# Kernel tuning notes

Hardware: AMD Instinct MI355X
Metric: run time of the kernel (lower is better)

The kernel has to match this reference:

```python
import jax, jax.numpy as jnp
import numpy as np

B, T, D = 4, 4096, 1024
N_DOCS, TOP_K, HEADS = 4096, 8, 4
EPS = 1e-12  # matches F.normalize default eps


def setup_inputs() -> dict:
    key = jax.random.key(0)
    ks = jax.random.split(key, 14)
    f = jnp.float32
    s = D ** -0.5
    return {
        "x": jax.random.normal(ks[0], (B, T, D), f),
        "hex_weights": jax.random.normal(ks[1], (B, T, 64), f),
        "doc_keys": jax.random.normal(ks[2], (N_DOCS, 64), f) * 0.1,
        "doc_values": jax.random.normal(ks[3], (N_DOCS, D), f) * 0.1,
        "Wq_hex": jax.random.normal(ks[4], (64, 64), f) * 0.125,
        "Wq": jax.random.normal(ks[5], (D, D), f) * s,
        "Wk": jax.random.normal(ks[6], (D, D), f) * s,
        "Wv": jax.random.normal(ks[7], (D, D), f) * s,
        "bq": jnp.zeros((D,), f),
        "bk": jnp.zeros((D,), f),
        "bv": jnp.zeros((D,), f),
        "Wo": jax.random.normal(ks[8], (D, D), f) * s,
        "bo": jnp.zeros((D,), f),
        "W_doc": jax.random.normal(ks[9], (D, D), f) * s,
        "gate": jnp.zeros((1,), f),
    }


def _l2norm(v):
    return v / jnp.maximum(jnp.linalg.norm(v, axis=-1, keepdims=True), EPS)


def reference(x, hex_weights, doc_keys, doc_values, Wq_hex, Wq, Wk, Wv,
              bq, bk, bv, Wo, bo, W_doc, gate):
    # --- retrieve: cosine similarity in 64-dim hexagram space ---
    q = hex_weights @ Wq_hex                      # (B,T,64)
    sim = jnp.einsum('bth,nh->btn', _l2norm(q), _l2norm(doc_keys))  # (B,T,N_DOCS)
    top_scores, top_idx = jax.lax.top_k(sim, TOP_K)  # (B,T,K)

    # --- gather + softmax-weighted combine ---
    doc_vals = doc_values[top_idx]                # (B,T,K,D) irregular gather
    attn_w = jax.nn.softmax(top_scores, axis=-1)  # (B,T,K)
    retrieved = jnp.einsum('btk,btkd->btd', attn_w, doc_vals)  # (B,T,D)
    doc_context = retrieved @ W_doc               # (B,T,D)

    # --- degenerate cross-attention: q len 1, kv len 1 per token ---
    # softmax over a single key is exactly 1, so attention output = v;
    # q/k projections contribute nothing (and have zero gradient), matching torch.
    v = doc_context @ Wv + bv                     # (B,T,D)
    out = v @ Wo + bo                             # out_proj

    return x + jax.nn.sigmoid(gate) * out
```

## Files before the change

### kernel.cpp

```cpp
#include <hip/hip_runtime.h>
#include <math.h>

#define NTOK  16384
#define DDIM  1024
#define NDOCS 4096
#define NSLICE 8
#define SLICE (NDOCS/NSLICE)
#define TOPL  6
#define KPT   64
#define MN20  (1u<<20)

typedef __attribute__((ext_vector_type(8))) short short8;
typedef __attribute__((ext_vector_type(4))) float f32x4;

__device__ __forceinline__ float b2f(unsigned short u){
  union { unsigned int i; float f; } v; v.i = ((unsigned int)u) << 16; return v.f;
}
__device__ __forceinline__ unsigned short f2b(float f){
  union { float f; unsigned int i; } v; v.f = f;
  unsigned int r = v.i + 0x7fffu + ((v.i >> 16) & 1u);
  return (unsigned short)(r >> 16);
}
__device__ __forceinline__ void gld16(const void* g, void* l){
  __builtin_amdgcn_global_load_lds(
      (const __attribute__((address_space(1))) void*)g,
      (__attribute__((address_space(3))) void*)l, 16, 0, 0);
}
__device__ __forceinline__ void kinsert(unsigned int* keys, unsigned int key){
  #pragma unroll
  for (int k = TOPL-1; k >= 1; --k){
    unsigned int lo = keys[k-1] < key ? keys[k-1] : key;
    keys[k] = keys[k] > lo ? keys[k] : lo;
  }
  keys[0] = keys[0] > key ? keys[0] : key;
}
__device__ __forceinline__ void ceswap(unsigned int& a, unsigned int& b){
  unsigned int mx = a > b ? a : b, mn = a > b ? b : a; a = mx; b = mn;
}
__device__ __forceinline__ void bitonic8(unsigned int* c){
  ceswap(c[0],c[4]); ceswap(c[1],c[5]); ceswap(c[2],c[6]); ceswap(c[3],c[7]);
  ceswap(c[0],c[2]); ceswap(c[1],c[3]); ceswap(c[4],c[6]); ceswap(c[5],c[7]);
  ceswap(c[0],c[1]); ceswap(c[2],c[3]); ceswap(c[4],c[5]); ceswap(c[6],c[7]);
}

__global__ __launch_bounds__(256)
void prep_kernel(const float* __restrict__ dvals, unsigned short* __restrict__ dv16,
                 const float* __restrict__ Wdoc,  unsigned short* __restrict__ wd16,
                 const float* __restrict__ Wv,    unsigned short* __restrict__ T1,
                 const float* __restrict__ Wo,    unsigned short* __restrict__ T2,
                 const float* __restrict__ bv, const float* __restrict__ bo,
                 float* __restrict__ bc){
  __shared__ unsigned short t[32][33];
  __shared__ float part[4][64];
  int bx = blockIdx.x, tid = threadIdx.x;
  if (bx < 5120){
    const float* in        = bx < 4096 ? dvals : Wdoc;
    unsigned short* outp   = bx < 4096 ? dv16  : wd16;
    size_t base = (size_t)(bx < 4096 ? bx : bx - 4096) * 1024;
    size_t i = base + (size_t)tid * 4;
    float4 v = *(const float4*)(in + i);
    ushort4 o; o.x = f2b(v.x); o.y = f2b(v.y); o.z = f2b(v.z); o.w = f2b(v.w);
    *(ushort4*)(outp + i) = o;
  } else if (bx < 7168){
    int b = bx - 5120;
    const float* in      = b < 1024 ? Wv : Wo;
    unsigned short* outp = b < 1024 ? T1 : T2;
    b &= 1023;
    int c0 = (b & 31) * 32, r0 = (b >> 5) * 32;
    int lc = tid & 31, lr = tid >> 5;
    #pragma unroll
    for (int i = 0; i < 4; i++){
      int r = lr + i*8;
      t[r][lc] = f2b(in[(size_t)(r0 + r)*DDIM + c0 + lc]);
    }
    __syncthreads();
    #pragma unroll
    for (int i = 0; i < 4; i++){
      int r = lr + i*8;
      outp[(size_t)(c0 + r)*DDIM + r0 + lc] = t[lc][r];
    }
  } else {
    int b = bx - 7168;
    int lane = tid & 63, w = tid >> 6;
    int n = b * 64 + lane;
    float acc = 0.f;
    int k0 = w * 256;
    for (int k = k0; k < k0 + 256; k++)
      acc += bv[k] * Wo[(size_t)k*DDIM + n];
    part[w][lane] = acc;
    __syncthreads();
    if (w == 0)
      bc[n] = part[0][lane] + part[1][lane] + part[2][lane] + part[3][lane] + bo[n];
  }
}

__global__ __launch_bounds__(256)
void norm_kernel(const float* __restrict__ hexw, const float* __restrict__ Wq,
                 float* __restrict__ qn, const float* __restrict__ dkeys,
                 float* __restrict__ dkn, unsigned short* __restrict__ dkn16s){
  __shared__ float Wsh[64*64];
  __shared__ float hx[4][64];
  int bx = blockIdx.x, tid = threadIdx.x;
  int w = tid >> 6, j = tid & 63;
  if (bx < 4096){
    #pragma unroll
    for (int i = 0; i < 16; i++){ int e = tid + i*256; Wsh[e] = Wq[e]; }
    int t = bx * 4 + w;
    hx[w][j] = hexw[(size_t)t*64 + j];
    __syncthreads();
    float s = 0.f;
    #pragma unroll
    for (int h = 0; h < 64; h++) s += hx[w][h] * Wsh[h*64 + j];
    float ss = s*s;
    #pragma unroll
    for (int off = 32; off >= 1; off >>= 1) ss += __shfl_xor(ss, off, 64);
    qn[(size_t)t*64 + j] = s / fmaxf(sqrtf(ss), 1e-12f);
  } else {
    int t = (bx - 4096) * 4 + w;
    float v = dkeys[(size_t)t*64 + j];
    float ss = v*v;
    #pragma unroll
    for (int off = 32; off >= 1; off >>= 1) ss += __shfl_xor(ss, off, 64);
    float o = v / fmaxf(sqrtf(ss), 1e-12f);
    dkn[(size_t)t*64 + j] = o;
    dkn16s[((size_t)(t >> 5) << 11) + ((j >> 3) << 8) + ((t & 31) << 3) + (j & 7)] = f2b(o);
  }
}

__global__ __launch_bounds__(256)
void topk_part(const float* __restrict__ qn, const unsigned short* __restrict__ dkn16s,
               unsigned int* __restrict__ kbuf){
  __shared__ __align__(16) unsigned short buf[2][2048];
  int tid  = threadIdx.x;
  int wv   = tid >> 6;
  int lane = tid & 63;
  int tl   = lane & 15;
  int g    = lane >> 4;
  int token = blockIdx.x*64 + wv*16 + tl;
  int dbase = blockIdx.y * SLICE;
  int T0    = dbase >> 5;

  const float* qrow = qn + (size_t)token*64 + g*8;
  float4 u0 = *(const float4*)(qrow);
  float4 u1 = *(const float4*)(qrow + 4);
  float4 v0 = *(const float4*)(qrow + 32);
  float4 v1 = *(const float4*)(qrow + 36);
  short8 q0 = (short8){(short)f2b(u0.x),(short)f2b(u0.y),(short)f2b(u0.z),(short)f2b(u0.w),
                       (short)f2b(u1.x),(short)f2b(u1.y),(short)f2b(u1.z),(short)f2b(u1.w)};
  short8 q1 = (short8){(short)f2b(v0.x),(short)f2b(v0.y),(short)f2b(v0.z),(short)f2b(v0.w),
                       (short)f2b(v1.x),(short)f2b(v1.y),(short)f2b(v1.z),(short)f2b(v1.w)};

  unsigned int keysA[TOPL], keysB[TOPL];
  #pragma unroll
  for (int k = 0; k < TOPL; k++){ keysA[k] = 0u; keysB[k] = 0u; }
  const unsigned int HI = 0xFFFF0000u;
  unsigned int idlow0 = 4095u - (unsigned)(dbase + g*4);

  gld16(dkn16s + ((size_t)T0 << 11) + wv*512 + lane*8, &buf[0][wv*512]);
  __syncthreads();

  #pragma unroll 2
  for (int it = 0; it < SLICE/32; ++it){
    int cur = it & 1;
    if (it < SLICE/32 - 1)
      gld16(dkn16s + ((size_t)(T0 + it + 1) << 11) + wv*512 + lane*8,
            &buf[cur ^ 1][wv*512]);

    const unsigned short* bp = &buf[cur][0];
    short8 a0 = *(const short8*)(bp + g*256        + tl*8);
    short8 a1 = *(const short8*)(bp + (g+4)*256    + tl*8);
    short8 b0 = *(const short8*)(bp + g*256 + 128  + tl*8);
    short8 b1 = *(const short8*)(bp + (g+4)*256 + 128 + tl*8);

    f32x4 accA = (f32x4){3.0f, 3.0f, 3.0f, 3.0f};
    f32x4 accB = (f32x4){3.0f, 3.0f, 3.0f, 3.0f};
    accA = __builtin_amdgcn_mfma_f32_16x16x32_bf16(a0, q0, accA, 0, 0, 0);
    accB = __builtin_amdgcn_mfma_f32_16x16x32_bf16(b0, q0, accB, 0, 0, 0);
    accA = __builtin_amdgcn_mfma_f32_16x16x32_bf16(a1, q1, accA, 0, 0, 0);
    accB = __builtin_amdgcn_mfma_f32_16x16x32_bf16(b1, q1, accB, 0, 0, 0);

    unsigned int ibA = idlow0 - (unsigned)(it*32);
    unsigned int ibB = ibA - 16u;
    #pragma unroll
    for (int r = 0; r < 4; ++r){
      unsigned int kA = (((__float_as_uint(accA[r]) << 8) - 0xC0000000u) & HI)
                      | (ibA - (unsigned)r);
      unsigned int kB = (((__float_as_uint(accB[r]) << 8) - 0xC0000000u) & HI)
                      | (ibB - (unsigned)r);
      kinsert(keysA, kA);
      kinsert(keysB, kB);
    }
    __syncthreads();
  }

  #pragma unroll
  for (int k = 0; k < TOPL; ++k) kinsert(keysA, keysB[k]);

  unsigned int pb[TOPL], c[8];
  #pragma unroll
  for (int j = 0; j < TOPL; ++j) pb[j] = __shfl_xor(keysA[j], 16, 64);
  c[0] = keysA[0];
  c[1] = keysA[1];
  c[2] = keysA[2] > pb[5] ? keysA[2] : pb[5];
  c[3] = keysA[3] > pb[4] ? keysA[3] : pb[4];
  c[4] = keysA[4] > pb[3] ? keysA[4] : pb[3];
  c[5] = keysA[5] > pb[2] ? keysA[5] : pb[2];
  c[6] = pb[1];
  c[7] = pb[0];
  bitonic8(c);
  unsigned int pc[8], d[8];
  #pragma unroll
  for (int j = 0; j < 8; ++j) pc[j] = __shfl_xor(c[j], 32, 64);
  #pragma unroll
  for (int j = 0; j < 8; ++j) d[j] = c[j] > pc[7-j] ? c[j] : pc[7-j];
  bitonic8(d);

  if (g == 0){
    size_t base = (size_t)token*KPT + (size_t)blockIdx.y*8;
    *(uint4*)&kbuf[base]     = (uint4){d[0], d[1], d[2], d[3]};
    *(uint4*)&kbuf[base + 4] = (uint4){d[4], d[5], d[6], d[7]};
  }
}

__global__ __launch_bounds__(256)
void topk_rescore(const unsigned int* __restrict__ kbuf, const float* __restrict__ qn,
                  const float* __restrict__ dkn, float* __restrict__ wsm,
                  int* __restrict__ idx){
  __shared__ unsigned int smid[4][16];
  __shared__ float       ssc[4][16];
  int tid = threadIdx.x, wv = tid >> 6, lane = tid & 63;
  int t = blockIdx.x * 4 + wv;

  unsigned int k = kbuf[(size_t)t*KPT + lane];
  int rank = 0;
  #pragma unroll
  for (int i = 0; i < 64; ++i){
    unsigned int o = __shfl(k, i, 64);
    rank += (o > k) ? 1 : 0;
  }
  if (rank < 16) smid[wv][rank] = k;
  __syncthreads();

  int cnum = lane >> 2, sub = lane & 3;
  unsigned int mk = smid[wv][cnum];
  int did = 4095 - (int)(mk & 0xFFFFu);
  const float4* kr = (const float4*)(dkn + (size_t)did*64 + sub*16);
  const float4* qp = (const float4*)(qn  + (size_t)t*64   + sub*16);
  float s = 0.f;
  #pragma unroll
  for (int c = 0; c < 4; ++c){
    float4 kv = kr[c], qv = qp[c];
    s += qv.x*kv.x + qv.y*kv.y + qv.z*kv.z + qv.w*kv.w;
  }
  s += __shfl_xor(s, 1, 64);
  s += __shfl_xor(s, 2, 64);
  if (sub == 0) ssc[wv][cnum] = s;
  __syncthreads();

  float sc = (lane < 16) ? ssc[wv][lane] : -1e30f;
  int   id = (lane < 16) ? (4095 - (int)(smid[wv][lane] & 0xFFFFu)) : 0x7fffffff;
  int r2 = 0;
  #pragma unroll
  for (int i = 0; i < 16; ++i){
    float os = __shfl(sc, i, 64);
    int   oi = __shfl(id, i, 64);
    r2 += (os > sc || (os == sc && oi < id)) ? 1 : 0;
  }
  float mx = sc;
  #pragma unroll
  for (int off = 1; off < 64; off <<= 1) mx = fmaxf(mx, __shfl_xor(mx, off, 64));
  float e = (lane < 16 && r2 < 8) ? expf(sc - mx) : 0.f;
  float sum = e;
  #pragma unroll
  for (int off = 1; off < 64; off <<= 1) sum += __shfl_xor(sum, off, 64);
  if (lane < 16 && r2 < 8){
    float inv = 1.f / sum;
    wsm[(size_t)t*8 + r2] = e * inv;
    idx[(size_t)t*8 + r2] = id;
  }
}

template<int TSTORE, int PARTIAL>
__global__ __launch_bounds__(256)
void gemm_bt_kernel(const unsigned short* __restrict__ A, const unsigned short* __restrict__ Bt,
                    void* __restrict__ C, int M, int N, int K){
  __shared__ __align__(16) short As[128*32];
  __shared__ __align__(16) short Bs[128*32];
  int tid  = threadIdx.x;
  int lane = tid & 63;
  int wv   = tid >> 6;
  int wm = wv & 1, wn = wv >> 1;
  size_t bm = (size_t)blockIdx.x * 128, bn = (size_t)blockIdx.y * 128;
  int klen = K / (int)gridDim.z;
  int kz0  = (int)blockIdx.z * klen;

  f32x4 acc[4][4];
  #pragma unroll
  for (int i = 0; i < 4; i++)
    #pragma unroll
    for (int j = 0; j < 4; j++) acc[i][j] = (f32x4){0.f, 0.f, 0.f, 0.f};

  size_t aoff = (bm + (size_t)(tid >> 2))*K + (tid & 3)*8 + kz0;
  size_t boff = (bn + (size_t)(tid >> 2))*K + (tid & 3)*8 + kz0;

  for (int k0 = 0; k0 < klen; k0 += 32){
    __syncthreads();
    gld16(A  + aoff + k0,                 &As[wv*512]);
    gld16(A  + aoff + (size_t)64*K + k0,  &As[2048 + wv*512]);
    gld16(Bt + boff + k0,                 &Bs[wv*512]);
    gld16(Bt + boff + (size_t)64*K + k0,  &Bs[2048 + wv*512]);
    __syncthreads();

    short8 af[4], bf[4];
    int kb = (lane >> 4) * 8;
    int rA = wm*64 + (lane & 15);
    int rB = wn*64 + (lane & 15);
    #pragma unroll
    for (int i = 0; i < 4; i++) af[i] = *(const short8*)&As[(rA + i*16)*32 + kb];
    #pragma unroll
    for (int i = 0; i < 4; i++) bf[i] = *(const short8*)&Bs[(rB + i*16)*32 + kb];
    #pragma unroll
    for (int i = 0; i < 4; i++)
      #pragma unroll
      for (int j = 0; j < 4; j++)
        acc[i][j] = __builtin_amdgcn_mfma_f32_16x16x32_bf16(af[i], bf[j], acc[i][j], 0, 0, 0);
  }

  int ci = lane & 15, rg = lane >> 4;
  #pragma unroll
  for (int i = 0; i < 4; i++)
    #pragma unroll
    for (int j = 0; j < 4; j++)
      #pragma unroll
      for (int r = 0; r < 4; r++){
        size_t row = bm + wm*64 + i*16 + rg*4 + r;
        size_t col = bn + wn*64 + j*16 + ci;
        size_t e = TSTORE ? (col*(size_t)M + row) : (row*(size_t)N + col);
        if (PARTIAL) ((float*)C)[(size_t)blockIdx.z*M*N + e] = acc[i][j][r];
        else         ((unsigned short*)C)[e] = f2b(acc[i][j][r]);
      }
}

__global__ __launch_bounds__(256)
void reduce4_bf16(const float* __restrict__ p, unsigned short* __restrict__ o){
  size_t i = ((size_t)blockIdx.x * 256 + threadIdx.x) * 4;
  float4 a0 = *(const float4*)(p + i);
  float4 a1 = *(const float4*)(p + i + (size_t)MN20);
  float4 a2 = *(const float4*)(p + i + (size_t)2*MN20);
  float4 a3 = *(const float4*)(p + i + (size_t)3*MN20);
  ushort4 r;
  r.x = f2b(a0.x + a1.x + a2.x + a3.x);
  r.y = f2b(a0.y + a1.y + a2.y + a3.y);
  r.z = f2b(a0.z + a1.z + a2.z + a3.z);
  r.w = f2b(a0.w + a1.w + a2.w + a3.w);
  *(ushort4*)(o + i) = r;
}

__global__ __launch_bounds__(256)
void output_kernel(const float* __restrict__ x, const float* __restrict__ wsm,
                   const int* __restrict__ idx, const unsigned short* __restrict__ P,
                   const float* __restrict__ bc, const float* __restrict__ gate,
                   float* __restrict__ out){
  __shared__ float ws8[2][8]; __shared__ int is8[2][8];
  int tid = threadIdx.x;
  int t0 = blockIdx.x * 2;
  if (tid < 16){
    int tt = tid >> 3, kk = tid & 7;
    ws8[tt][kk] = wsm[(size_t)(t0 + tt)*8 + kk];
    int ii = idx[(size_t)(t0 + tt)*8 + kk];
    is8[tt][kk] = ii < 0 ? 0 : (ii > NDOCS-1 ? NDOCS-1 : ii);
  }
  __syncthreads();
  float g = 1.f / (1.f + expf(-gate[0]));
  int tt = tid >> 7;
  int t  = t0 + tt;
  int c  = (tid & 127) * 8;
  float a[8] = {0.f,0.f,0.f,0.f,0.f,0.f,0.f,0.f};
  #pragma unroll
  for (int k = 0; k < 8; k++){
    short8 u = *(const short8*)(P + (size_t)is8[tt][k]*DDIM + c);
    float w = ws8[tt][k];
    #pragma unroll
    for (int j = 0; j < 8; j++) a[j] += w * b2f((unsigned short)u[j]);
  }
  const f32x4* xp = (const f32x4*)(x + (size_t)t*DDIM + c);
  f32x4 xf0 = __builtin_nontemporal_load(xp);
  f32x4 xf1 = __builtin_nontemporal_load(xp + 1);
  const f32x4* bp = (const f32x4*)(bc + c);
  f32x4 b0 = bp[0], b1 = bp[1];
  f32x4 o0, o1;
  #pragma unroll
  for (int j = 0; j < 4; j++){
    o0[j] = xf0[j] + g * (a[j]     + b0[j]);
    o1[j] = xf1[j] + g * (a[j + 4] + b1[j]);
  }
  f32x4* op = (f32x4*)(out + (size_t)t*DDIM + c);
  __builtin_nontemporal_store(o0, op);
  __builtin_nontemporal_store(o1, op + 1);
}

__global__ __launch_bounds__(256)
void zero_out_kernel(float* __restrict__ out){
  size_t i = ((size_t)blockIdx.x * 256 + threadIdx.x) * 4;
  *(float4*)(out + i) = (float4){0.f,0.f,0.f,0.f};
}

extern "C" void kernel_launch(void* const* d_in, const int* in_sizes, int n_in,
                              void* d_out, int out_size, void* d_ws, size_t ws_size,
                              hipStream_t stream){
  (void)in_sizes; (void)n_in; (void)out_size;
  const float* x     = (const float*)d_in[0];
  const float* hexw  = (const float*)d_in[1];
  const float* dkeys = (const float*)d_in[2];
  const float* dvals = (const float*)d_in[3];
  const float* Wqh   = (const float*)d_in[4];
  const float* Wv    = (const float*)d_in[7];
  const float* bv    = (const float*)d_in[10];
  const float* Wo    = (const float*)d_in[11];
  const float* bo    = (const float*)d_in[12];
  const float* Wdoc  = (const float*)d_in[13];
  const float* gate  = (const float*)d_in[14];
  float* out = (float*)d_out;

  const size_t NEED = ((size_t)22 << 20) + 4096;
  if (ws_size < NEED){
    zero_out_kernel<<<NTOK*DDIM/1024, 256, 0, stream>>>(out);
    return;
  }

  char* ws = (char*)d_ws;
  float* qn             = (float*)(ws);
  float* dkn            = (float*)(ws + ((size_t)4 << 20));
  float* wsm            = (float*)(ws + ((size_t)5 << 20));
  int*   idx            = (int*)  (ws + ((size_t)5 << 20) + (512 << 10));
  unsigned short* T1    = (unsigned short*)(ws + ((size_t)6  << 20));
  unsigned short* T2    = (unsigned short*)(ws + ((size_t)8  << 20));
  unsigned short* tmp   = (unsigned short*)(ws + ((size_t)10 << 20));
  unsigned short* WcT   = (unsigned short*)(ws + ((size_t)12 << 20));
  unsigned short* P     = (unsigned short*)(ws + ((size_t)14 << 20));
  unsigned short* dkn16s= (unsigned short*)(ws + ((size_t)12 << 20));
  float* bc             = (float*)(ws + ((size_t)22 << 20));
  char* dob             = (char*)d_out;
  float*          pbuf = (float*)dob;
  unsigned int*   kbuf = (unsigned int*)dob;
  unsigned short* dv16 = (unsigned short*)(dob + ((size_t)16 << 20));
  unsigned short* wd16 = (unsigned short*)(dob + ((size_t)24 << 20));

  prep_kernel<<<7184, 256, 0, stream>>>(dvals, dv16, Wdoc, wd16, Wv, T1, Wo, T2,
                                        bv, bo, bc);
  gemm_bt_kernel<0,1><<<dim3(8,8,4),  256, 0, stream>>>(wd16, T1, pbuf, DDIM, DDIM, DDIM);
  reduce4_bf16<<<1024, 256, 0, stream>>>(pbuf, tmp);
  gemm_bt_kernel<1,1><<<dim3(8,8,4),  256, 0, stream>>>(tmp,  T2, pbuf, DDIM, DDIM, DDIM);
  reduce4_bf16<<<1024, 256, 0, stream>>>(pbuf, WcT);
  gemm_bt_kernel<0,0><<<dim3(32,8,1), 256, 0, stream>>>(dv16, WcT, P, NDOCS, DDIM, DDIM);

  norm_kernel<<<4096 + NDOCS/4, 256, 0, stream>>>(hexw, Wqh, qn, dkeys, dkn, dkn16s);
  topk_part<<<dim3(NTOK/64, NSLICE), 256, 0, stream>>>(qn, dkn16s, kbuf);
  topk_rescore<<<NTOK/4, 256, 0, stream>>>(kbuf, qn, dkn, wsm, idx);

  output_kernel<<<NTOK/2, 256, 0, stream>>>(x, wsm, idx, P, bc, gate, out);
}
```

Before: 333.7 us.

## Co-schedule weight GEMMs with top-k stages in merged kernel launches

The small weight-folding GEMMs run in the same launches as the independent retrieval stages. The first split-K GEMM shares a launch with the partial top-k search, the doc-projection GEMM shares one with the rescore, and the norm work is folded into the prep kernel. This lets the under-occupied 256-block GEMMs overlap with the token-parallel work and cuts the number of launches. To allow that overlap, kbuf moves to its own region of the output buffer instead of aliasing pbuf. The output kernel also switches from nontemporal to ordinary loads and stores. Merging bodies raises the per-block LDS footprint to the largest branch, which may reduce occupancy for the lighter branches.

```diff
diff --git a/kernel.cpp b/kernel.cpp
--- a/kernel.cpp
+++ b/kernel.cpp
@@ -43,15 +43,229 @@
   ceswap(c[0],c[1]); ceswap(c[2],c[3]); ceswap(c[4],c[5]); ceswap(c[6],c[7]);
 }
 
-__global__ __launch_bounds__(256)
-void prep_kernel(const float* __restrict__ dvals, unsigned short* __restrict__ dv16,
+template<int PARTIAL>
+__device__ __forceinline__ void gemm_body(
+    const unsigned short* __restrict__ A, const unsigned short* __restrict__ Bt,
+    void* __restrict__ C, int M, int N, int K, int klen, int kz0, size_t zoff,
+    int bxg, int byg, short* As, short* Bs){
+  int tid  = threadIdx.x;
+  int lane = tid & 63;
+  int wv   = tid >> 6;
+  int wm = wv & 1, wn = wv >> 1;
+  size_t bm = (size_t)bxg * 128, bn = (size_t)byg * 128;
+
+  f32x4 acc[4][4];
+  #pragma unroll
+  for (int i = 0; i < 4; i++)
+    #pragma unroll
+    for (int j = 0; j < 4; j++) acc[i][j] = (f32x4){0.f, 0.f, 0.f, 0.f};
+
+  size_t aoff = (bm + (size_t)(tid >> 2))*K + (tid & 3)*8 + kz0;
+  size_t boff = (bn + (size_t)(tid >> 2))*K + (tid & 3)*8 + kz0;
+
+  for (int k0 = 0; k0 < klen; k0 += 32){
+    __syncthreads();
+    gld16(A  + aoff + k0,                 &As[wv*512]);
+    gld16(A  + aoff + (size_t)64*K + k0,  &As[2048 + wv*512]);
+    gld16(Bt + boff + k0,                 &Bs[wv*512]);
+    gld16(Bt + boff + (size_t)64*K + k0,  &Bs[2048 + wv*512]);
+    __syncthreads();
+
+    short8 af[4], bf[4];
+    int kb = (lane >> 4) * 8;
+    int rA = wm*64 + (lane & 15);
+    int rB = wn*64 + (lane & 15);
+    #pragma unroll
+    for (int i = 0; i < 4; i++) af[i] = *(const short8*)&As[(rA + i*16)*32 + kb];
+    #pragma unroll
+    for (int i = 0; i < 4; i++) bf[i] = *(const short8*)&Bs[(rB + i*16)*32 + kb];
+    #pragma unroll
+    for (int i = 0; i < 4; i++)
+      #pragma unroll
+      for (int j = 0; j < 4; j++)
+        acc[i][j] = __builtin_amdgcn_mfma_f32_16x16x32_bf16(af[i], bf[j], acc[i][j], 0, 0, 0);
+  }
+
+  int ci = lane & 15, rg = lane >> 4;
+  #pragma unroll
+  for (int i = 0; i < 4; i++)
+    #pragma unroll
+    for (int j = 0; j < 4; j++)
+      #pragma unroll
+      for (int r = 0; r < 4; r++){
+        size_t row = bm + wm*64 + i*16 + rg*4 + r;
+        size_t col = bn + wn*64 + j*16 + ci;
+        size_t e = row*(size_t)N + col;
+        if (PARTIAL) ((float*)C)[zoff + e] = acc[i][j][r];
+        else         ((unsigned short*)C)[e] = f2b(acc[i][j][r]);
+      }
+}
+
+__device__ __forceinline__ void part_body(
+    int px, int py, const float* __restrict__ qn,
+    const unsigned short* __restrict__ dkn16s, unsigned int* __restrict__ kbuf,
+    unsigned short* buf){
+  int tid  = threadIdx.x;
+  int wv   = tid >> 6;
+  int lane = tid & 63;
+  int tl   = lane & 15;
+  int g    = lane >> 4;
+  int token = px*64 + wv*16 + tl;
+  int dbase = py * SLICE;
+  int T0    = dbase >> 5;
+
+  const float* qrow = qn + (size_t)token*64 + g*8;
+  float4 u0 = *(const float4*)(qrow);
+  float4 u1 = *(const float4*)(qrow + 4);
+  float4 v0 = *(const float4*)(qrow + 32);
+  float4 v1 = *(const float4*)(qrow + 36);
+  short8 q0 = (short8){(short)f2b(u0.x),(short)f2b(u0.y),(short)f2b(u0.z),(short)f2b(u0.w),
+                       (short)f2b(u1.x),(short)f2b(u1.y),(short)f2b(u1.z),(short)f2b(u1.w)};
+  short8 q1 = (short8){(short)f2b(v0.x),(short)f2b(v0.y),(short)f2b(v0.z),(short)f2b(v0.w),
+                       (short)f2b(v1.x),(short)f2b(v1.y),(short)f2b(v1.z),(short)f2b(v1.w)};
+
+  unsigned int keysA[TOPL], keysB[TOPL];
+  #pragma unroll
+  for (int k = 0; k < TOPL; k++){ keysA[k] = 0u; keysB[k] = 0u; }
+  const unsigned int HI = 0xFFFF0000u;
+  unsigned int idlow0 = 4095u - (unsigned)(dbase + g*4);
+
+  gld16(dkn16s + ((size_t)T0 << 11) + wv*512 + lane*8, &buf[wv*512]);
+  __syncthreads();
+
+  #pragma unroll 2
+  for (int it = 0; it < SLICE/32; ++it){
+    int cur = it & 1;
+    if (it < SLICE/32 - 1)
+      gld16(dkn16s + ((size_t)(T0 + it + 1) << 11) + wv*512 + lane*8,
+            &buf[(cur ^ 1)*2048 + wv*512]);
+
+    const unsigned short* bp = &buf[cur*2048];
+    short8 a0 = *(const short8*)(bp + g*256        + tl*8);
+    short8 a1 = *(const short8*)(bp + (g+4)*256    + tl*8);
+    short8 b0 = *(const short8*)(bp + g*256 + 128  + tl*8);
+    short8 b1 = *(const short8*)(bp + (g+4)*256 + 128 + tl*8);
+
+    f32x4 accA = (f32x4){3.0f, 3.0f, 3.0f, 3.0f};
+    f32x4 accB = (f32x4){3.0f, 3.0f, 3.0f, 3.0f};
+    accA = __builtin_amdgcn_mfma_f32_16x16x32_bf16(a0, q0, accA, 0, 0, 0);
+    accB = __builtin_amdgcn_mfma_f32_16x16x32_bf16(b0, q0, accB, 0, 0, 0);
+    accA = __builtin_amdgcn_mfma_f32_16x16x32_bf16(a1, q1, accA, 0, 0, 0);
+    accB = __builtin_amdgcn_mfma_f32_16x16x32_bf16(b1, q1, accB, 0, 0, 0);
+
+    unsigned int ibA = idlow0 - (unsigned)(it*32);
+    unsigned int ibB = ibA - 16u;
+    #pragma unroll
+    for (int r = 0; r < 4; ++r){
+      unsigned int kA = (((__float_as_uint(accA[r]) << 8) - 0xC0000000u) & HI)
+                      | (ibA - (unsigned)r);
+      unsigned int kB = (((__float_as_uint(accB[r]) << 8) - 0xC0000000u) & HI)
+                      | (ibB - (unsigned)r);
+      kinsert(keysA, kA);
+      kinsert(keysB, kB);
+    }
+    __syncthreads();
+  }
+
+  #pragma unroll
+  for (int k = 0; k < TOPL; ++k) kinsert(keysA, keysB[k]);
+
+  unsigned int pb[TOPL], c[8];
+  #pragma unroll
+  for (int j = 0; j < TOPL; ++j) pb[j] = __shfl_xor(keysA[j], 16, 64);
+  c[0] = keysA[0];
+  c[1] = keysA[1];
+  c[2] = keysA[2] > pb[5] ? keysA[2] : pb[5];
+  c[3] = keysA[3] > pb[4] ? keysA[3] : pb[4];
+  c[4] = keysA[4] > pb[3] ? keysA[4] : pb[3];
+  c[5] = keysA[5] > pb[2] ? keysA[5] : pb[2];
+  c[6] = pb[1];
+  c[7] = pb[0];
+  bitonic8(c);
+  unsigned int pc[8], d[8];
+  #pragma unroll
+  for (int j = 0; j < 8; ++j) pc[j] = __shfl_xor(c[j], 32, 64);
+  #pragma unroll
+  for (int j = 0; j < 8; ++j) d[j] = c[j] > pc[7-j] ? c[j] : pc[7-j];
+  bitonic8(d);
+
+  if (g == 0){
+    size_t base = (size_t)token*KPT + (size_t)py*8;
+    *(uint4*)&kbuf[base]     = (uint4){d[0], d[1], d[2], d[3]};
+    *(uint4*)&kbuf[base + 4] = (uint4){d[4], d[5], d[6], d[7]};
+  }
+}
+
+__device__ __forceinline__ void rescore_body(
+    int b2, const unsigned int* __restrict__ kbuf, const float* __restrict__ qn,
+    const float* __restrict__ dkn, float* __restrict__ wsm, int* __restrict__ idx,
+    unsigned int* smid, float* ssc){
+  int tid = threadIdx.x, wv = tid >> 6, lane = tid & 63;
+  int t = b2 * 4 + wv;
+
+  unsigned int k = kbuf[(size_t)t*KPT + lane];
+  int rank = 0;
+  #pragma unroll
+  for (int i = 0; i < 64; ++i){
+    unsigned int o = __shfl(k, i, 64);
+    rank += (o > k) ? 1 : 0;
+  }
+  if (rank < 16) smid[wv*16 + rank] = k;
+  __syncthreads();
+
+  int cnum = lane >> 2, sub = lane & 3;
+  unsigned int mk = smid[wv*16 + cnum];
+  int did = 4095 - (int)(mk & 0xFFFFu);
+  const float4* kr = (const float4*)(dkn + (size_t)did*64 + sub*16);
+  const float4* qp = (const float4*)(qn  + (size_t)t*64   + sub*16);
+  float s = 0.f;
+  #pragma unroll
+  for (int c = 0; c < 4; ++c){
+    float4 kv = kr[c], qv = qp[c];
+    s += qv.x*kv.x + qv.y*kv.y + qv.z*kv.z + qv.w*kv.w;
+  }
+  s += __shfl_xor(s, 1, 64);
+  s += __shfl_xor(s, 2, 64);
+  if (sub == 0) ssc[wv*16 + cnum] = s;
+  __syncthreads();
+
+  float sc = (lane < 16) ? ssc[wv*16 + lane] : -1e30f;
+  int   id = (lane < 16) ? (4095 - (int)(smid[wv*16 + lane] & 0xFFFFu)) : 0x7fffffff;
+  int r2 = 0;
+  #pragma unroll
+  for (int i = 0; i < 16; ++i){
+    float os = __shfl(sc, i, 64);
+    int   oi = __shfl(id, i, 64);
+    r2 += (os > sc || (os == sc && oi < id)) ? 1 : 0;
+  }
+  float mx = sc;
+  #pragma unroll
+  for (int off = 1; off < 64; off <<= 1) mx = fmaxf(mx, __shfl_xor(mx, off, 64));
+  float e = (lane < 16 && r2 < 8) ? expf(sc - mx) : 0.f;
+  float sum = e;
+  #pragma unroll
+  for (int off = 1; off < 64; off <<= 1) sum += __shfl_xor(sum, off, 64);
+  if (lane < 16 && r2 < 8){
+    float inv = 1.f / sum;
+    wsm[(size_t)t*8 + r2] = e * inv;
+    idx[(size_t)t*8 + r2] = id;
+  }
+}
+
+__global__ __launch_bounds__(256)
+void prep_norm_kernel(const float* __restrict__ dvals, unsigned short* __restrict__ dv16,
                  const float* __restrict__ Wdoc,  unsigned short* __restrict__ wd16,
                  const float* __restrict__ Wv,    unsigned short* __restrict__ T1,
                  const float* __restrict__ Wo,    unsigned short* __restrict__ T2,
                  const float* __restrict__ bv, const float* __restrict__ bo,
-                 float* __restrict__ bc){
+                 float* __restrict__ bc,
+                 const float* __restrict__ hexw, const float* __restrict__ Wq,
+                 float* __restrict__ qn, const float* __restrict__ dkeys,
+                 float* __restrict__ dkn, unsigned short* __restrict__ dkn16s){
   __shared__ unsigned short t[32][33];
   __shared__ float part[4][64];
+  __shared__ float Wsh[64*64];
+  __shared__ float hx[4][64];
   int bx = blockIdx.x, tid = threadIdx.x;
   if (bx < 5120){
     const float* in        = bx < 4096 ? dvals : Wdoc;
@@ -79,7 +293,7 @@
       int r = lr + i*8;
       outp[(size_t)(c0 + r)*DDIM + r0 + lc] = t[lc][r];
     }
-  } else {
+  } else if (bx < 7184){
     int b = bx - 7168;
     int lane = tid & 63, w = tid >> 6;
     int n = b * 64 + lane;
@@ -91,22 +305,13 @@
     __syncthreads();
     if (w == 0)
       bc[n] = part[0][lane] + part[1][lane] + part[2][lane] + part[3][lane] + bo[n];
-  }
-}
-
-__global__ __launch_bounds__(256)
-void norm_kernel(const float* __restrict__ hexw, const float* __restrict__ Wq,
-                 float* __restrict__ qn, const float* __restrict__ dkeys,
-                 float* __restrict__ dkn, unsigned short* __restrict__ dkn16s){
-  __shared__ float Wsh[64*64];
-  __shared__ float hx[4][64];
-  int bx = blockIdx.x, tid = threadIdx.x;
-  int w = tid >> 6, j = tid & 63;
-  if (bx < 4096){
+  } else if (bx < 11280){
+    int b = bx - 7184;
+    int w = tid >> 6, j = tid & 63;
     #pragma unroll
     for (int i = 0; i < 16; i++){ int e = tid + i*256; Wsh[e] = Wq[e]; }
-    int t = bx * 4 + w;
-    hx[w][j] = hexw[(size_t)t*64 + j];
+    int tt = b * 4 + w;
+    hx[w][j] = hexw[(size_t)tt*64 + j];
     __syncthreads();
     float s = 0.f;
     #pragma unroll
@@ -114,195 +319,56 @@
     float ss = s*s;
     #pragma unroll
     for (int off = 32; off >= 1; off >>= 1) ss += __shfl_xor(ss, off, 64);
-    qn[(size_t)t*64 + j] = s / fmaxf(sqrtf(ss), 1e-12f);
+    qn[(size_t)tt*64 + j] = s / fmaxf(sqrtf(ss), 1e-12f);
   } else {
-    int t = (bx - 4096) * 4 + w;
-    float v = dkeys[(size_t)t*64 + j];
+    int b = bx - 11280;
+    int w = tid >> 6, j = tid & 63;
+    int tt = b * 4 + w;
+    float v = dkeys[(size_t)tt*64 + j];
     float ss = v*v;
     #pragma unroll
     for (int off = 32; off >= 1; off >>= 1) ss += __shfl_xor(ss, off, 64);
     float o = v / fmaxf(sqrtf(ss), 1e-12f);
-    dkn[(size_t)t*64 + j] = o;
-    dkn16s[((size_t)(t >> 5) << 11) + ((j >> 3) << 8) + ((t & 31) << 3) + (j & 7)] = f2b(o);
-  }
-}
-
-__global__ __launch_bounds__(256)
-void topk_part(const float* __restrict__ qn, const unsigned short* __restrict__ dkn16s,
-               unsigned int* __restrict__ kbuf){
-  __shared__ __align__(16) unsigned short buf[2][2048];
-  int tid  = threadIdx.x;
-  int wv   = tid >> 6;
-  int lane = tid & 63;
-  int tl   = lane & 15;
-  int g    = lane >> 4;
-  int token = blockIdx.x*64 + wv*16 + tl;
-  int dbase = blockIdx.y * SLICE;
-  int T0    = dbase >> 5;
-
-  const float* qrow = qn + (size_t)token*64 + g*8;
-  float4 u0 = *(const float4*)(qrow);
-  float4 u1 = *(const float4*)(qrow + 4);
-  float4 v0 = *(const float4*)(qrow + 32);
-  float4 v1 = *(const float4*)(qrow + 36);
-  short8 q0 = (short8){(short)f2b(u0.x),(short)f2b(u0.y),(short)f2b(u0.z),(short)f2b(u0.w),
-                       (short)f2b(u1.x),(short)f2b(u1.y),(short)f2b(u1.z),(short)f2b(u1.w)};
-  short8 q1 = (short8){(short)f2b(v0.x),(short)f2b(v0.y),(short)f2b(v0.z),(short)f2b(v0.w),
-                       (short)f2b(v1.x),(short)f2b(v1.y),(short)f2b(v1.z),(short)f2b(v1.w)};
-
-  unsigned int keysA[TOPL], keysB[TOPL];
-  #pragma unroll
-  for (int k = 0; k < TOPL; k++){ keysA[k] = 0u; keysB[k] = 0u; }
-  const unsigned int HI = 0xFFFF0000u;
-  unsigned int idlow0 = 4095u - (unsigned)(dbase + g*4);
-
-  gld16(dkn16s + ((size_t)T0 << 11) + wv*512 + lane*8, &buf[0][wv*512]);
-  __syncthreads();
-
-  #pragma unroll 2
-  for (int it = 0; it < SLICE/32; ++it){
-    int cur = it & 1;
-    if (it < SLICE/32 - 1)
-      gld16(dkn16s + ((size_t)(T0 + it + 1) << 11) + wv*512 + lane*8,
-            &buf[cur ^ 1][wv*512]);
-
-    const unsigned short* bp = &buf[cur][0];
-    short8 a0 = *(const short8*)(bp + g*256        + tl*8);
-    short8 a1 = *(const short8*)(bp + (g+4)*256    + tl*8);
-    short8 b0 = *(const short8*)(bp + g*256 + 128  + tl*8);
-    short8 b1 = *(const short8*)(bp + (g+4)*256 + 128 + tl*8);
-
-    f32x4 accA = (f32x4){3.0f, 3.0f, 3.0f, 3.0f};
-    f32x4 accB = (f32x4){3.0f, 3.0f, 3.0f, 3.0f};
-    accA = __builtin_amdgcn_mfma_f32_16x16x32_bf16(a0, q0, accA, 0, 0, 0);
-    accB = __builtin_amdgcn_mfma_f32_16x16x32_bf16(b0, q0, accB, 0, 0, 0);
-    accA = __builtin_amdgcn_mfma_f32_16x16x32_bf16(a1, q1, accA, 0, 0, 0);
-    accB = __builtin_amdgcn_mfma_f32_16x16x32_bf16(b1, q1, accB, 0, 0, 0);
-
-    unsigned int ibA = idlow0 - (unsigned)(it*32);
-    unsigned int ibB = ibA - 16u;
-    #pragma unroll
-    for (int r = 0; r < 4; ++r){
-      unsigned int kA = (((__float_as_uint(accA[r]) << 8) - 0xC0000000u) & HI)
-                      | (ibA - (unsigned)r);
-      unsigned int kB = (((__float_as_uint(accB[r]) << 8) - 0xC0000000u) & HI)
-                      | (ibB - (unsigned)r);
-      kinsert(keysA, kA);
-      kinsert(keysB, kB);
-    }
-    __syncthreads();
-  }
-
-  #pragma unroll
-  for (int k = 0; k < TOPL; ++k) kinsert(keysA, keysB[k]);
-
-  unsigned int pb[TOPL], c[8];
-  #pragma unroll
-  for (int j = 0; j < TOPL; ++j) pb[j] = __shfl_xor(keysA[j], 16, 64);
-  c[0] = keysA[0];
-  c[1] = keysA[1];
-  c[2] = keysA[2] > pb[5] ? keysA[2] : pb[5];
-  c[3] = keysA[3] > pb[4] ? keysA[3] : pb[4];
-  c[4] = keysA[4] > pb[3] ? keysA[4] : pb[3];
-  c[5] = keysA[5] > pb[2] ? keysA[5] : pb[2];
-  c[6] = pb[1];
-  c[7] = pb[0];
-  bitonic8(c);
-  unsigned int pc[8], d[8];
-  #pragma unroll
-  for (int j = 0; j < 8; ++j) pc[j] = __shfl_xor(c[j], 32, 64);
-  #pragma unroll
-  for (int j = 0; j < 8; ++j) d[j] = c[j] > pc[7-j] ? c[j] : pc[7-j];
-  bitonic8(d);
-
-  if (g == 0){
-    size_t base = (size_t)token*KPT + (size_t)blockIdx.y*8;
-    *(uint4*)&kbuf[base]     = (uint4){d[0], d[1], d[2], d[3]};
-    *(uint4*)&kbuf[base + 4] = (uint4){d[4], d[5], d[6], d[7]};
-  }
-}
-
-__global__ __launch_bounds__(256)
-void topk_rescore(const unsigned int* __restrict__ kbuf, const float* __restrict__ qn,
-                  const float* __restrict__ dkn, float* __restrict__ wsm,
-                  int* __restrict__ idx){
-  __shared__ unsigned int smid[4][16];
-  __shared__ float       ssc[4][16];
-  int tid = threadIdx.x, wv = tid >> 6, lane = tid & 63;
-  int t = blockIdx.x * 4 + wv;
-
-  unsigned int k = kbuf[(size_t)t*KPT + lane];
-  int rank = 0;
-  #pragma unroll
-  for (int i = 0; i < 64; ++i){
-    unsigned int o = __shfl(k, i, 64);
-    rank += (o > k) ? 1 : 0;
-  }
-  if (rank < 16) smid[wv][rank] = k;
-  __syncthreads();
-
-  int cnum = lane >> 2, sub = lane & 3;
-  unsigned int mk = smid[wv][cnum];
-  int did = 4095 - (int)(mk & 0xFFFFu);
-  const float4* kr = (const float4*)(dkn + (size_t)did*64 + sub*16);
-  const float4* qp = (const float4*)(qn  + (size_t)t*64   + sub*16);
-  float s = 0.f;
-  #pragma unroll
-  for (int c = 0; c < 4; ++c){
-    float4 kv = kr[c], qv = qp[c];
-    s += qv.x*kv.x + qv.y*kv.y + qv.z*kv.z + qv.w*kv.w;
-  }
-  s += __shfl_xor(s, 1, 64);
-  s += __shfl_xor(s, 2, 64);
-  if (sub == 0) ssc[wv][cnum] = s;
-  __syncthreads();
-
-  float sc = (lane < 16) ? ssc[wv][lane] : -1e30f;
-  int   id = (lane < 16) ? (4095 - (int)(smid[wv][lane] & 0xFFFFu)) : 0x7fffffff;
-  int r2 = 0;
-  #pragma unroll
-  for (int i = 0; i < 16; ++i){
-    float os = __shfl(sc, i, 64);
-    int   oi = __shfl(id, i, 64);
-    r2 += (os > sc || (os == sc && oi < id)) ? 1 : 0;
-  }
-  float mx = sc;
-  #pragma unroll
-  for (int off = 1; off < 64; off <<= 1) mx = fmaxf(mx, __shfl_xor(mx, off, 64));
-  float e = (lane < 16 && r2 < 8) ? expf(sc - mx) : 0.f;
-  float sum = e;
-  #pragma unroll
-  for (int off = 1; off < 64; off <<= 1) sum += __shfl_xor(sum, off, 64);
-  if (lane < 16 && r2 < 8){
-    float inv = 1.f / sum;
-    wsm[(size_t)t*8 + r2] = e * inv;
-    idx[(size_t)t*8 + r2] = id;
-  }
-}
-
-template<int TSTORE, int PARTIAL>
-__global__ __launch_bounds__(256)
-void gemm_bt_kernel(const unsigned short* __restrict__ A, const unsigned short* __restrict__ Bt,
-                    void* __restrict__ C, int M, int N, int K){
-  __shared__ __align__(16) short As[128*32];
-  __shared__ __align__(16) short Bs[128*32];
-  int tid  = threadIdx.x;
-  int lane = tid & 63;
-  int wv   = tid >> 6;
+    dkn[(size_t)tt*64 + j] = o;
+    dkn16s[((size_t)(tt >> 5) << 11) + ((j >> 3) << 8) + ((tt & 31) << 3) + (j & 7)] = f2b(o);
+  }
+}
+
+__global__ __launch_bounds__(256)
+void g1_part_kernel(const unsigned short* __restrict__ A, const unsigned short* __restrict__ Bt,
+                    float* __restrict__ pbuf, const float* __restrict__ qn,
+                    const unsigned short* __restrict__ dkn16s, unsigned int* __restrict__ kbuf){
+  __shared__ __align__(16) short lds[8192];
+  int b = blockIdx.x;
+  if (b < 256){
+    int bz = b >> 6, rem = b & 63;
+    gemm_body<1>(A, Bt, pbuf, DDIM, DDIM, DDIM, 256, bz*256, (size_t)bz*MN20,
+                 rem & 7, rem >> 3, lds, lds + 4096);
+  } else {
+    int b2 = b - 256;
+    part_body(b2 & 255, b2 >> 8, qn, dkn16s, kbuf, (unsigned short*)lds);
+  }
+}
+
+__global__ __launch_bounds__(256)
+void g2_kernel(const unsigned short* __restrict__ A, const unsigned short* __restrict__ Bt,
+               float* __restrict__ C){
+  __shared__ __align__(16) short lds[8192];
+  int b = blockIdx.x;
+  int bz = b >> 6, rem = b & 63;
+  int bxg = rem & 7, byg = rem >> 3;
+  short* As = lds; short* Bs = lds + 4096;
+  int tid = threadIdx.x, lane = tid & 63, wv = tid >> 6;
   int wm = wv & 1, wn = wv >> 1;
-  size_t bm = (size_t)blockIdx.x * 128, bn = (size_t)blockIdx.y * 128;
-  int klen = K / (int)gridDim.z;
-  int kz0  = (int)blockIdx.z * klen;
-
+  size_t bm = (size_t)bxg * 128, bn = (size_t)byg * 128;
+  int K = DDIM, klen = 256, kz0 = bz * 256;
   f32x4 acc[4][4];
   #pragma unroll
   for (int i = 0; i < 4; i++)
     #pragma unroll
-    for (int j = 0; j < 4; j++) acc[i][j] = (f32x4){0.f, 0.f, 0.f, 0.f};
-
+    for (int j = 0; j < 4; j++) acc[i][j] = (f32x4){0.f,0.f,0.f,0.f};
   size_t aoff = (bm + (size_t)(tid >> 2))*K + (tid & 3)*8 + kz0;
   size_t boff = (bn + (size_t)(tid >> 2))*K + (tid & 3)*8 + kz0;
-
   for (int k0 = 0; k0 < klen; k0 += 32){
     __syncthreads();
     gld16(A  + aoff + k0,                 &As[wv*512]);
@@ -310,7 +376,6 @@
     gld16(Bt + boff + k0,                 &Bs[wv*512]);
     gld16(Bt + boff + (size_t)64*K + k0,  &Bs[2048 + wv*512]);
     __syncthreads();
-
     short8 af[4], bf[4];
     int kb = (lane >> 4) * 8;
     int rA = wm*64 + (lane & 15);
@@ -325,7 +390,6 @@
       for (int j = 0; j < 4; j++)
         acc[i][j] = __builtin_amdgcn_mfma_f32_16x16x32_bf16(af[i], bf[j], acc[i][j], 0, 0, 0);
   }
-
   int ci = lane & 15, rg = lane >> 4;
   #pragma unroll
   for (int i = 0; i < 4; i++)
@@ -335,10 +399,26 @@
       for (int r = 0; r < 4; r++){
         size_t row = bm + wm*64 + i*16 + rg*4 + r;
         size_t col = bn + wn*64 + j*16 + ci;
-        size_t e = TSTORE ? (col*(size_t)M + row) : (row*(size_t)N + col);
-        if (PARTIAL) ((float*)C)[(size_t)blockIdx.z*M*N + e] = acc[i][j][r];
-        else         ((unsigned short*)C)[e] = f2b(acc[i][j][r]);
+        C[(size_t)bz*MN20 + col*(size_t)DDIM + row] = acc[i][j][r];
       }
+}
+
+__global__ __launch_bounds__(256)
+void g3_rescore_kernel(const unsigned short* __restrict__ dv16,
+                       const unsigned short* __restrict__ WcT,
+                       unsigned short* __restrict__ P,
+                       const unsigned int* __restrict__ kbuf,
+                       const float* __restrict__ qn, const float* __restrict__ dkn,
+                       float* __restrict__ wsm, int* __restrict__ idx){
+  __shared__ __align__(16) short lds[8192];
+  int b = blockIdx.x;
+  if (b < 256){
+    gemm_body<0>(dv16, WcT, P, NDOCS, DDIM, DDIM, DDIM, 0, 0,
+                 b & 31, b >> 5, lds, lds + 4096);
+  } else {
+    rescore_body(b - 256, kbuf, qn, dkn, wsm, idx,
+                 (unsigned int*)lds, (float*)((char*)lds + 256));
+  }
 }
 
 __global__ __launch_bounds__(256)
@@ -384,8 +464,8 @@
     for (int j = 0; j < 8; j++) a[j] += w * b2f((unsigned short)u[j]);
   }
   const f32x4* xp = (const f32x4*)(x + (size_t)t*DDIM + c);
-  f32x4 xf0 = __builtin_nontemporal_load(xp);
-  f32x4 xf1 = __builtin_nontemporal_load(xp + 1);
+  f32x4 xf0 = xp[0];
+  f32x4 xf1 = xp[1];
   const f32x4* bp = (const f32x4*)(bc + c);
   f32x4 b0 = bp[0], b1 = bp[1];
   f32x4 o0, o1;
@@ -395,8 +475,8 @@
     o1[j] = xf1[j] + g * (a[j + 4] + b1[j]);
   }
   f32x4* op = (f32x4*)(out + (size_t)t*DDIM + c);
-  __builtin_nontemporal_store(o0, op);
-  __builtin_nontemporal_store(o1, op + 1);
+  op[0] = o0;
+  op[1] = o1;
 }
 
 __global__ __launch_bounds__(256)
@@ -437,26 +517,21 @@
   unsigned short* T2    = (unsigned short*)(ws + ((size_t)8  << 20));
   unsigned short* tmp   = (unsigned short*)(ws + ((size_t)10 << 20));
   unsigned short* WcT   = (unsigned short*)(ws + ((size_t)12 << 20));
+  unsigned short* dkn16s= (unsigned short*)(ws + ((size_t)12 << 20));
   unsigned short* P     = (unsigned short*)(ws + ((size_t)14 << 20));
-  unsigned short* dkn16s= (unsigned short*)(ws + ((size_t)12 << 20));
   float* bc             = (float*)(ws + ((size_t)22 << 20));
   char* dob             = (char*)d_out;
   float*          pbuf = (float*)dob;
-  unsigned int*   kbuf = (unsigned int*)dob;
   unsigned short* dv16 = (unsigned short*)(dob + ((size_t)16 << 20));
   unsigned short* wd16 = (unsigned short*)(dob + ((size_t)24 << 20));
-
-  prep_kernel<<<7184, 256, 0, stream>>>(dvals, dv16, Wdoc, wd16, Wv, T1, Wo, T2,
-                                        bv, bo, bc);
-  gemm_bt_kernel<0,1><<<dim3(8,8,4),  256, 0, stream>>>(wd16, T1, pbuf, DDIM, DDIM, DDIM);
+  unsigned int*   kbuf = (unsigned int*)(dob + ((size_t)26 << 20));
+
+  prep_norm_kernel<<<12304, 256, 0, stream>>>(dvals, dv16, Wdoc, wd16, Wv, T1, Wo, T2,
+                                              bv, bo, bc, hexw, Wqh, qn, dkeys, dkn, dkn16s);
+  g1_part_kernel<<<256 + 2048, 256, 0, stream>>>(wd16, T1, pbuf, qn, dkn16s, kbuf);
   reduce4_bf16<<<1024, 256, 0, stream>>>(pbuf, tmp);
-  gemm_bt_kernel<1,1><<<dim3(8,8,4),  256, 0, stream>>>(tmp,  T2, pbuf, DDIM, DDIM, DDIM);
+  g2_kernel<<<256, 256, 0, stream>>>(tmp, T2, pbuf);
   reduce4_bf16<<<1024, 256, 0, stream>>>(pbuf, WcT);
-  gemm_bt_kernel<0,0><<<dim3(32,8,1), 256, 0, stream>>>(dv16, WcT, P, NDOCS, DDIM, DDIM);
-
-  norm_kernel<<<4096 + NDOCS/4, 256, 0, stream>>>(hexw, Wqh, qn, dkeys, dkn, dkn16s);
-  topk_part<<<dim3(NTOK/64, NSLICE), 256, 0, stream>>>(qn, dkn16s, kbuf);
-  topk_rescore<<<NTOK/4, 256, 0, stream>>>(kbuf, qn, dkn, wsm, idx);
-
+  g3_rescore_kernel<<<256 + 4096, 256, 0, stream>>>(dv16, WcT, P, kbuf, qn, dkn, wsm, idx);
   output_kernel<<<NTOK/2, 256, 0, stream>>>(x, wsm, idx, P, bc, gate, out);
 }
```

Measured after the change: 303.3 us. -9.1%, faster.
